# Optimization experiments

Measured on AMD Instinct MI355X. Metric: run time of the kernel, lower is better.

## Reference

```python
import jax, jax.numpy as jnp
import numpy as np
import math

H = 16
DQ = 64
NEG = -1000000000.0


def setup_inputs() -> dict:
    key = jax.random.key(0)
    ks = jax.random.split(key, 8)
    B, S, D = 2, 2048, 1024
    scale = 1.0 / math.sqrt(D)
    return {
        "embedding": jax.random.normal(ks[0], (B, S, D), dtype=jnp.float32),
        "mask": jax.random.randint(ks[1], (B, 1, S), 0, 2, dtype=jnp.int32),
        "Wq": jax.random.normal(ks[2], (D, D), dtype=jnp.float32) * scale,
        "bq": jnp.zeros((D,), dtype=jnp.float32),
        "Wk": jax.random.normal(ks[3], (D, D), dtype=jnp.float32) * scale,
        "bk": jnp.zeros((D,), dtype=jnp.float32),
        "Wv": jax.random.normal(ks[4], (D, D), dtype=jnp.float32) * scale,
        "bv": jnp.zeros((D,), dtype=jnp.float32),
        "Wo": jax.random.normal(ks[5], (D, D), dtype=jnp.float32) * scale,
        "bo": jnp.zeros((D,), dtype=jnp.float32),
    }


def reference(embedding, mask, Wq, bq, Wk, bk, Wv, bv, Wo, bo):
    B, S, D = embedding.shape
    # projections -> [B, H, S, DQ]
    def proj(W, b):
        return (embedding @ W + b).reshape(B, S, H, DQ).transpose(0, 2, 1, 3)
    q, k, v = proj(Wq, bq), proj(Wk, bk), proj(Wv, bv)
    scores = jnp.einsum("bhqd,bhkd->bhqk", q, k) / math.sqrt(DQ)
    m = mask[:, None]  # [B,1,1,S] broadcasts over heads and query positions
    scores = jnp.where(m == 0, NEG, scores)
    attn = jax.nn.softmax(scores, axis=-1)
    x = jnp.einsum("bhqk,bhkd->bhqd", attn, v)
    x = x.transpose(0, 2, 1, 3).reshape(B, S, H * DQ)
    return x @ Wo + bo
```

## Files before the change

### kernel.cpp

```cpp
#include <hip/hip_runtime.h>
#include <stdint.h>

#define B_ 2
#define S_ 2048
#define D_ 1024
#define H_ 16
#define DQ_ 64
#define M_ 4096

typedef unsigned short ushort_t;
typedef __attribute__((ext_vector_type(8))) short short8;
typedef __attribute__((ext_vector_type(4))) float floatx4;
typedef __attribute__((ext_vector_type(16))) float floatx16;

#if __has_builtin(__builtin_amdgcn_exp2f)
#define EXP2(x) __builtin_amdgcn_exp2f(x)
#else
#define EXP2(x) exp2f(x)
#endif

__device__ __forceinline__ ushort_t f2bf(float f) {
  union { float f; uint32_t u; } v; v.f = f;
  uint32_t r = v.u + 0x7FFFu + ((v.u >> 16) & 1u);
  return (ushort_t)(r >> 16);
}

__device__ __forceinline__ uint32_t pk2_trunc(float a, float b) {
  union { float f; uint32_t u; } va, vb; va.f = a; vb.f = b;
  return (va.u >> 16) | (vb.u & 0xFFFF0000u);
}
__device__ __forceinline__ uint32_t pk2_rne(float a, float b) {
  return (uint32_t)f2bf(a) | ((uint32_t)f2bf(b) << 16);
}

__device__ __forceinline__ void async16(const ushort_t* g, ushort_t* l) {
  __builtin_amdgcn_global_load_lds(
      (const __attribute__((address_space(1))) uint32_t*)g,
      (__attribute__((address_space(3))) uint32_t*)l, 16, 0, 0);
}

__global__ void k_prep(const float* __restrict__ emb, const float* __restrict__ Wq,
                       const float* __restrict__ Wk, const float* __restrict__ Wv,
                       const float* __restrict__ Wo, const int* __restrict__ mask,
                       ushort_t* __restrict__ embb, ushort_t* __restrict__ Wt,
                       int* __restrict__ pos, ushort_t* __restrict__ biasC,
                       int* __restrict__ cntp) {
  __shared__ float t[32][33];
  int blk = blockIdx.x, tid = threadIdx.x;
  if (blk < 4096) {
    int i = (blk * 256 + tid) * 4;
    float4 v = *(const float4*)(emb + i);
    uint64_t pk = (uint64_t)f2bf(v.x) | ((uint64_t)f2bf(v.y) << 16) |
                  ((uint64_t)f2bf(v.z) << 32) | ((uint64_t)f2bf(v.w) << 48);
    *(uint64_t*)(embb + i) = pk;
  } else if (blk < 8192) {
    int widx = blk - 4096;
    int z = widx >> 10, tt = widx & 1023;
    const float* W = (z == 0) ? Wq : (z == 1) ? Wk : (z == 2) ? Wv : Wo;
    ushort_t* out = Wt + (size_t)z * D_ * D_;
    int k0 = (tt >> 5) * 32, n0 = (tt & 31) * 32;
    int tx = tid & 31, ty = tid >> 5;
    for (int r = 0; r < 32; r += 8)
      t[ty + r][tx] = W[(size_t)(k0 + ty + r) * D_ + n0 + tx];
    __syncthreads();
    for (int r = 0; r < 32; r += 8)
      out[(size_t)(n0 + ty + r) * D_ + k0 + tx] = f2bf(t[tx][ty + r]);
  } else if (tid < 64) {
    int b = blk - 8192, lane = tid;
    int base = 0;
    for (int c = 0; c < 32; c++) {
      int s = c * 64 + lane;
      bool m = mask[b * S_ + s] != 0;
      unsigned long long bits = __ballot(m);
      int pre = base + __popcll(bits & ((1ull << lane) - 1ull));
      pos[b * S_ + s] = m ? pre : -1;
      base += __popcll(bits);
    }
    int cnt = base;
    for (int c = 0; c < 32; c++) {
      int i = c * 64 + lane;
      biasC[b * S_ + i] = (i < cnt) ? (ushort_t)0xC180 : (ushort_t)0xCE6E;
    }
    if (lane == 0) cntp[b] = (cnt + 63) & ~63;
  }
}

template <int IM>
__device__ __forceinline__ void gemm_core2(const ushort_t* __restrict__ A,
                                           const ushort_t* __restrict__ Bt,
                                           ushort_t* As, ushort_t* Bs,
                                           int m0, int n0, floatx4 (&acc)[IM][4]) {
  int t = threadIdx.x, lane = t & 63, w = t >> 6;
  int wm = (w >> 1) * (IM * 16), wn = (w & 1) * 64;
  int l15 = lane & 15, quad = lane >> 4;
  int srow8 = (lane >> 3) & 7;
  int sch = ((lane & 7) ^ srow8) * 8;
  const ushort_t* Ag = A + (size_t)(m0 + w * 8 + srow8) * D_ + sch;
  const ushort_t* Bg = Bt + (size_t)(n0 + w * 8 + srow8) * D_ + sch;
  for (int kt = 0; kt < D_; kt += 64) {
    __syncthreads();
#pragma unroll
    for (int c = 0; c < IM; c++)
      async16(Ag + kt + (size_t)c * 32 * D_, As + (c * 32 + w * 8) * 64);
#pragma unroll
    for (int c = 0; c < 4; c++)
      async16(Bg + kt + (size_t)c * 32 * D_, Bs + (c * 32 + w * 8) * 64);
    __syncthreads();
#pragma unroll
    for (int ks = 0; ks < 2; ks++) {
      int ch = ((ks * 4 + quad) ^ (l15 & 7)) * 8;
      short8 a[IM], b[4];
#pragma unroll
      for (int i = 0; i < IM; i++)
        a[i] = *(const short8*)(As + (wm + i * 16 + l15) * 64 + ch);
#pragma unroll
      for (int j = 0; j < 4; j++)
        b[j] = *(const short8*)(Bs + (wn + j * 16 + l15) * 64 + ch);
#pragma unroll
      for (int i = 0; i < IM; i++)
#pragma unroll
        for (int j = 0; j < 4; j++)
          acc[i][j] = __builtin_amdgcn_mfma_f32_16x16x32_bf16(a[i], b[j], acc[i][j], 0, 0, 0);
    }
  }
}

__global__ __launch_bounds__(256, 3) void k_proj(
    const ushort_t* __restrict__ A, const ushort_t* __restrict__ Wt,
    const float* __restrict__ bq, const float* __restrict__ bk,
    const float* __restrict__ bv, const int* __restrict__ pos,
    ushort_t* __restrict__ Q, ushort_t* __restrict__ K, ushort_t* __restrict__ V) {
  __shared__ __align__(16) ushort_t As[128 * 64];
  __shared__ __align__(16) ushort_t Bs[128 * 64];
  int z = blockIdx.z;
  const ushort_t* Bt = Wt + (size_t)z * D_ * D_;
  const float* bias = (z == 0) ? bq : (z == 1) ? bk : bv;
  int m0 = blockIdx.x * 128, n0 = blockIdx.y * 128;
  floatx4 acc[4][4] = {};
  gemm_core2<4>(A, Bt, As, Bs, m0, n0, acc);
  int lane = threadIdx.x & 63, w = threadIdx.x >> 6;
  int wm = (w >> 1) * 64, wn = (w & 1) * 64;
  int quad = lane >> 4, l15 = lane & 15;
  float scale = 0.125f * 1.44269504f;
#pragma unroll
  for (int i = 0; i < 4; i++)
#pragma unroll
    for (int j = 0; j < 4; j++) {
      int ncol = n0 + wn + j * 16 + l15;
      float bb = bias[ncol];
      int h = ncol >> 6, dq = ncol & 63;
      int m = m0 + wm + i * 16 + quad * 4;
      int b = m >> 11, s = m & (S_ - 1);
      if (z == 0) {
#pragma unroll
        for (int r = 0; r < 4; r++)
          Q[((size_t)(b * H_ + h) * S_ + (s + r)) * DQ_ + dq] =
              f2bf((acc[i][j][r] + bb) * scale);
      } else {
        int4 p4 = *(const int4*)(pos + b * S_ + s);
#pragma unroll
        for (int r = 0; r < 4; r++) {
          int ps = (&p4.x)[r];
          if (ps >= 0) {
            float v = acc[i][j][r] + bb;
            if (z == 1) K[((size_t)(b * H_ + h) * S_ + ps) * DQ_ + dq] = f2bf(v);
            else        V[((size_t)(b * H_ + h) * DQ_ + dq) * S_ + ps] = f2bf(v);
          }
        }
      }
    }
}

__global__ __launch_bounds__(256, 2) void k_attn(
    const ushort_t* __restrict__ Q, const ushort_t* __restrict__ Kc,
    const ushort_t* __restrict__ Vc, const ushort_t* __restrict__ biasC,
    const int* __restrict__ cntp, ushort_t* __restrict__ X) {
  int bh = blockIdx.y, b = bh >> 4, h = bh & 15;
  int t = threadIdx.x, lane = t & 63, w = t >> 6;
  int l31 = lane & 31, hi = lane >> 5;
  int q0 = blockIdx.x * 128 + w * 32;
  const ushort_t* Qh = Q + (size_t)bh * S_ * DQ_;
  const ushort_t* Kh = Kc + (size_t)bh * S_ * DQ_;
  const ushort_t* Vh = Vc + (size_t)bh * DQ_ * S_;
  const ushort_t* bbp = biasC + b * S_;
  int nk = cntp[b];

  __shared__ __align__(16) ushort_t Ks[64 * 64];
  __shared__ __align__(16) ushort_t Vs[64 * 64];

  short8 qf[4];
#pragma unroll
  for (int ks = 0; ks < 4; ks++)
    qf[ks] = *(const short8*)(Qh + (size_t)(q0 + l31) * DQ_ + ks * 16 + hi * 8);

  short8 qb = {};
  qb[0] = hi ? (short)0 : (short)0x3F80;

  int srow8 = (lane >> 3) & 7;
  int sch = ((lane & 7) ^ srow8) * 8;
  const ushort_t* Kg1 = Kh + (size_t)(w * 8 + srow8) * DQ_ + sch;
  const ushort_t* Vg1 = Vh + (size_t)(w * 8 + srow8) * S_ + sch;

  floatx16 o[2] = {};
  float lsum = 0.0f;

  for (int k0 = 0; k0 < nk; k0 += 64) {
    __syncthreads();
    async16(Kg1 + (size_t)k0 * DQ_, Ks + w * 512);
    async16(Kg1 + (size_t)(k0 + 32) * DQ_, Ks + w * 512 + 2048);
    async16(Vg1 + k0, Vs + w * 512);
    async16(Vg1 + (size_t)32 * S_ + k0, Vs + w * 512 + 2048);
    ushort_t bv0 = bbp[k0 + l31], bv1 = bbp[k0 + 32 + l31];
    __syncthreads();

    floatx16 s0 = {}, s1 = {};
#pragma unroll
    for (int ks = 0; ks < 4; ks++) {
      int ch = ((ks * 2 + hi) ^ (l31 & 7)) * 8;
      short8 kf0 = *(const short8*)(Ks + l31 * 64 + ch);
      short8 kf1 = *(const short8*)(Ks + (32 + l31) * 64 + ch);
      s0 = __builtin_amdgcn_mfma_f32_32x32x16_bf16(kf0, qf[ks], s0, 0, 0, 0);
      s1 = __builtin_amdgcn_mfma_f32_32x32x16_bf16(kf1, qf[ks], s1, 0, 0, 0);
    }
    short8 kb0 = {}, kb1 = {};
    kb0[0] = hi ? (short)0 : (short)bv0;
    kb1[0] = hi ? (short)0 : (short)bv1;
    s0 = __builtin_amdgcn_mfma_f32_32x32x16_bf16(kb0, qb, s0, 0, 0, 0);
    s1 = __builtin_amdgcn_mfma_f32_32x32x16_bf16(kb1, qb, s1, 0, 0, 0);

    uint32_t pk[2][4][2];
#pragma unroll
    for (int g = 0; g < 4; g++) {
      float p0[4], p1[4];
#pragma unroll
      for (int j = 0; j < 4; j++) {
        p0[j] = EXP2(s0[g * 4 + j]);
        p1[j] = EXP2(s1[g * 4 + j]);
        lsum += p0[j] + p1[j];
      }
      pk[0][g][0] = pk2_trunc(p0[0], p0[1]); pk[0][g][1] = pk2_trunc(p0[2], p0[3]);
      pk[1][g][0] = pk2_trunc(p1[0], p1[1]); pk[1][g][1] = pk2_trunc(p1[2], p1[3]);
    }

#pragma unroll
    for (int ks = 0; ks < 4; ks++) {
      int a = ks >> 1, gb = (ks & 1) * 2;
      uint32_t pass0 = hi ? pk[a][gb][0]     : pk[a][gb + 1][0];
      uint32_t pass1 = hi ? pk[a][gb][1]     : pk[a][gb + 1][1];
      uint32_t own0  = hi ? pk[a][gb + 1][0] : pk[a][gb][0];
      uint32_t own1  = hi ? pk[a][gb + 1][1] : pk[a][gb][1];
      uint32_t recv0 = __shfl_xor(pass0, 32, 64);
      uint32_t recv1 = __shfl_xor(pass1, 32, 64);
      union { uint32_t u[4]; short8 v; } pf;
      pf.u[0] = hi ? recv0 : own0;
      pf.u[1] = hi ? recv1 : own1;
      pf.u[2] = hi ? own0 : recv0;
      pf.u[3] = hi ? own1 : recv1;
      int ch = ((ks * 2 + hi) ^ (l31 & 7)) * 8;
      short8 vf0 = *(const short8*)(Vs + l31 * 64 + ch);
      short8 vf1 = *(const short8*)(Vs + (32 + l31) * 64 + ch);
      o[0] = __builtin_amdgcn_mfma_f32_32x32x16_bf16(vf0, pf.v, o[0], 0, 0, 0);
      o[1] = __builtin_amdgcn_mfma_f32_32x32x16_bf16(vf1, pf.v, o[1], 0, 0, 0);
    }
  }

  float l = lsum + __shfl_xor(lsum, 32, 64);
  float inv = 1.0f / l;
  int q = q0 + l31;
  size_t base = (size_t)(b * S_ + q) * D_ + h * DQ_;
#pragma unroll
  for (int a = 0; a < 2; a++)
#pragma unroll
    for (int g = 0; g < 4; g++) {
      uint2 st;
      st.x = pk2_rne(o[a][4 * g] * inv, o[a][4 * g + 1] * inv);
      st.y = pk2_rne(o[a][4 * g + 2] * inv, o[a][4 * g + 3] * inv);
      *(uint2*)(X + base + a * 32 + g * 8 + 4 * hi) = st;
    }
}

__global__ __launch_bounds__(256, 2) void k_oproj(
    const ushort_t* __restrict__ A, const ushort_t* __restrict__ Wt,
    const float* __restrict__ bias, float* __restrict__ C) {
  __shared__ __align__(16) ushort_t As[64 * 64];
  __shared__ __align__(16) ushort_t Bs[128 * 64];
  int m0 = blockIdx.x * 64, n0 = blockIdx.y * 128;
  floatx4 acc[2][4] = {};
  gemm_core2<2>(A, Wt, As, Bs, m0, n0, acc);
  int lane = threadIdx.x & 63, w = threadIdx.x >> 6;
  int wm = (w >> 1) * 32, wn = (w & 1) * 64;
  int quad = lane >> 4, l15 = lane & 15;
#pragma unroll
  for (int i = 0; i < 2; i++)
#pragma unroll
    for (int j = 0; j < 4; j++) {
      int ncol = n0 + wn + j * 16 + l15;
      float bb = bias[ncol];
      int mr = m0 + wm + i * 16 + quad * 4;
#pragma unroll
      for (int r = 0; r < 4; r++)
        C[(size_t)(mr + r) * D_ + ncol] = acc[i][j][r] + bb;
    }
}

extern "C" void kernel_launch(void* const* d_in, const int* in_sizes, int n_in,
                              void* d_out, int out_size, void* d_ws, size_t ws_size,
                              hipStream_t stream) {
  const float* emb  = (const float*)d_in[0];
  const int*   mask = (const int*)d_in[1];
  const float* Wq = (const float*)d_in[2];
  const float* bq = (const float*)d_in[3];
  const float* Wk = (const float*)d_in[4];
  const float* bk = (const float*)d_in[5];
  const float* Wv = (const float*)d_in[6];
  const float* bv = (const float*)d_in[7];
  const float* Wo = (const float*)d_in[8];
  const float* bo = (const float*)d_in[9];
  float* out = (float*)d_out;

  ushort_t* embb  = (ushort_t*)d_ws;
  ushort_t* Wt    = embb + (size_t)M_ * D_;
  ushort_t* Qb    = Wt + (size_t)4 * D_ * D_;
  ushort_t* Kb    = Qb + (size_t)M_ * D_;
  ushort_t* Vb    = Kb + (size_t)M_ * D_;
  ushort_t* Xb    = Vb + (size_t)M_ * D_;
  ushort_t* biasC = Xb + (size_t)M_ * D_;
  int* pos        = (int*)(biasC + (size_t)B_ * S_);
  int* cntp       = pos + B_ * S_;

  k_prep<<<dim3(8192 + B_), 256, 0, stream>>>(emb, Wq, Wk, Wv, Wo, mask,
                                              embb, Wt, pos, biasC, cntp);
  k_proj<<<dim3(32, 8, 3), 256, 0, stream>>>(embb, Wt, bq, bk, bv, pos, Qb, Kb, Vb);
  k_attn<<<dim3(16, 32), 256, 0, stream>>>(Qb, Kb, Vb, biasC, cntp, Xb);
  k_oproj<<<dim3(64, 8), 256, 0, stream>>>(Xb, Wt + (size_t)3 * D_ * D_, bo, out);
}
```

Before: 178.6 us.

## Fuse all four kernels into one persistent cooperative kernel with grid syncs

Replaces the prep, projection, attention and output-projection launches with a single cooperative persistent kernel. Phases are separated by grid.sync() and each phase loops over virtual blocks. The goal is to remove launch gaps and kernel-boundary drain between the four stages. In exchange, every phase runs with the fused kernel's register and LDS budget and occupancy, grid barriers cost time, and host queries (occupancy, device properties) are added on every launch.

After: 358.3 us. 101% more time.

```diff
diff --git a/kernel.cpp b/kernel.cpp
--- a/kernel.cpp
+++ b/kernel.cpp
@@ -1,4 +1,5 @@
 #include <hip/hip_runtime.h>
+#include <hip/hip_cooperative_groups.h>
 #include <stdint.h>
 
 #define B_ 2
@@ -37,52 +38,6 @@
   __builtin_amdgcn_global_load_lds(
       (const __attribute__((address_space(1))) uint32_t*)g,
       (__attribute__((address_space(3))) uint32_t*)l, 16, 0, 0);
-}
-
-__global__ void k_prep(const float* __restrict__ emb, const float* __restrict__ Wq,
-                       const float* __restrict__ Wk, const float* __restrict__ Wv,
-                       const float* __restrict__ Wo, const int* __restrict__ mask,
-                       ushort_t* __restrict__ embb, ushort_t* __restrict__ Wt,
-                       int* __restrict__ pos, ushort_t* __restrict__ biasC,
-                       int* __restrict__ cntp) {
-  __shared__ float t[32][33];
-  int blk = blockIdx.x, tid = threadIdx.x;
-  if (blk < 4096) {
-    int i = (blk * 256 + tid) * 4;
-    float4 v = *(const float4*)(emb + i);
-    uint64_t pk = (uint64_t)f2bf(v.x) | ((uint64_t)f2bf(v.y) << 16) |
-                  ((uint64_t)f2bf(v.z) << 32) | ((uint64_t)f2bf(v.w) << 48);
-    *(uint64_t*)(embb + i) = pk;
-  } else if (blk < 8192) {
-    int widx = blk - 4096;
-    int z = widx >> 10, tt = widx & 1023;
-    const float* W = (z == 0) ? Wq : (z == 1) ? Wk : (z == 2) ? Wv : Wo;
-    ushort_t* out = Wt + (size_t)z * D_ * D_;
-    int k0 = (tt >> 5) * 32, n0 = (tt & 31) * 32;
-    int tx = tid & 31, ty = tid >> 5;
-    for (int r = 0; r < 32; r += 8)
-      t[ty + r][tx] = W[(size_t)(k0 + ty + r) * D_ + n0 + tx];
-    __syncthreads();
-    for (int r = 0; r < 32; r += 8)
-      out[(size_t)(n0 + ty + r) * D_ + k0 + tx] = f2bf(t[tx][ty + r]);
-  } else if (tid < 64) {
-    int b = blk - 8192, lane = tid;
-    int base = 0;
-    for (int c = 0; c < 32; c++) {
-      int s = c * 64 + lane;
-      bool m = mask[b * S_ + s] != 0;
-      unsigned long long bits = __ballot(m);
-      int pre = base + __popcll(bits & ((1ull << lane) - 1ull));
-      pos[b * S_ + s] = m ? pre : -1;
-      base += __popcll(bits);
-    }
-    int cnt = base;
-    for (int c = 0; c < 32; c++) {
-      int i = c * 64 + lane;
-      biasC[b * S_ + i] = (i < cnt) ? (ushort_t)0xC180 : (ushort_t)0xCE6E;
-    }
-    if (lane == 0) cntp[b] = (cnt + 63) & ~63;
-  }
 }
 
 template <int IM>
@@ -125,182 +80,240 @@
   }
 }
 
-__global__ __launch_bounds__(256, 3) void k_proj(
-    const ushort_t* __restrict__ A, const ushort_t* __restrict__ Wt,
+__global__ __launch_bounds__(256, 2) void k_fused(
+    const float* __restrict__ emb, const float* __restrict__ Wq,
+    const float* __restrict__ Wk, const float* __restrict__ Wv,
+    const float* __restrict__ Wo, const int* __restrict__ mask,
     const float* __restrict__ bq, const float* __restrict__ bk,
-    const float* __restrict__ bv, const int* __restrict__ pos,
-    ushort_t* __restrict__ Q, ushort_t* __restrict__ K, ushort_t* __restrict__ V) {
-  __shared__ __align__(16) ushort_t As[128 * 64];
-  __shared__ __align__(16) ushort_t Bs[128 * 64];
-  int z = blockIdx.z;
-  const ushort_t* Bt = Wt + (size_t)z * D_ * D_;
-  const float* bias = (z == 0) ? bq : (z == 1) ? bk : bv;
-  int m0 = blockIdx.x * 128, n0 = blockIdx.y * 128;
-  floatx4 acc[4][4] = {};
-  gemm_core2<4>(A, Bt, As, Bs, m0, n0, acc);
-  int lane = threadIdx.x & 63, w = threadIdx.x >> 6;
-  int wm = (w >> 1) * 64, wn = (w & 1) * 64;
-  int quad = lane >> 4, l15 = lane & 15;
-  float scale = 0.125f * 1.44269504f;
-#pragma unroll
-  for (int i = 0; i < 4; i++)
-#pragma unroll
-    for (int j = 0; j < 4; j++) {
-      int ncol = n0 + wn + j * 16 + l15;
-      float bb = bias[ncol];
-      int h = ncol >> 6, dq = ncol & 63;
-      int m = m0 + wm + i * 16 + quad * 4;
-      int b = m >> 11, s = m & (S_ - 1);
-      if (z == 0) {
-#pragma unroll
-        for (int r = 0; r < 4; r++)
-          Q[((size_t)(b * H_ + h) * S_ + (s + r)) * DQ_ + dq] =
-              f2bf((acc[i][j][r] + bb) * scale);
-      } else {
-        int4 p4 = *(const int4*)(pos + b * S_ + s);
-#pragma unroll
-        for (int r = 0; r < 4; r++) {
-          int ps = (&p4.x)[r];
-          if (ps >= 0) {
-            float v = acc[i][j][r] + bb;
-            if (z == 1) K[((size_t)(b * H_ + h) * S_ + ps) * DQ_ + dq] = f2bf(v);
-            else        V[((size_t)(b * H_ + h) * DQ_ + dq) * S_ + ps] = f2bf(v);
+    const float* __restrict__ bv, const float* __restrict__ bo,
+    float* __restrict__ out,
+    ushort_t* __restrict__ embb, ushort_t* __restrict__ Wt,
+    ushort_t* __restrict__ Qb, ushort_t* __restrict__ Kb,
+    ushort_t* __restrict__ Vb, ushort_t* __restrict__ Xb,
+    ushort_t* __restrict__ biasC, int* __restrict__ pos,
+    int* __restrict__ cntp) {
+  cooperative_groups::grid_group grid = cooperative_groups::this_grid();
+  __shared__ __align__(16) char smem[32768];
+  int tid = threadIdx.x, nb = gridDim.x;
+  int lane = tid & 63, w = tid >> 6;
+
+  for (int vb = blockIdx.x; vb < 8192 + B_; vb += nb) {
+    if (vb < 4096) {
+      int i = (vb * 256 + tid) * 4;
+      float4 v = *(const float4*)(emb + i);
+      uint64_t pk = (uint64_t)f2bf(v.x) | ((uint64_t)f2bf(v.y) << 16) |
+                    ((uint64_t)f2bf(v.z) << 32) | ((uint64_t)f2bf(v.w) << 48);
+      *(uint64_t*)(embb + i) = pk;
+    } else if (vb < 8192) {
+      float (*t)[33] = (float(*)[33])smem;
+      int widx = vb - 4096;
+      int z = widx >> 10, tt = widx & 1023;
+      const float* W = (z == 0) ? Wq : (z == 1) ? Wk : (z == 2) ? Wv : Wo;
+      ushort_t* o = Wt + (size_t)z * D_ * D_;
+      int k0 = (tt >> 5) * 32, n0 = (tt & 31) * 32;
+      int tx = tid & 31, ty = tid >> 5;
+      __syncthreads();
+      for (int r = 0; r < 32; r += 8)
+        t[ty + r][tx] = W[(size_t)(k0 + ty + r) * D_ + n0 + tx];
+      __syncthreads();
+      for (int r = 0; r < 32; r += 8)
+        o[(size_t)(n0 + ty + r) * D_ + k0 + tx] = f2bf(t[tx][ty + r]);
+    } else if (tid < 64) {
+      int b = vb - 8192;
+      int base = 0;
+      for (int c = 0; c < 32; c++) {
+        int s = c * 64 + tid;
+        bool m = mask[b * S_ + s] != 0;
+        unsigned long long bits = __ballot(m);
+        int pre = base + __popcll(bits & ((1ull << tid) - 1ull));
+        pos[b * S_ + s] = m ? pre : -1;
+        base += __popcll(bits);
+      }
+      int cnt = base;
+      for (int c = 0; c < 32; c++) {
+        int i = c * 64 + tid;
+        biasC[b * S_ + i] = (i < cnt) ? (ushort_t)0xC180 : (ushort_t)0xCE6E;
+      }
+      if (tid == 0) cntp[b] = (cnt + 63) & ~63;
+    }
+  }
+  grid.sync();
+
+  {
+    ushort_t* As = (ushort_t*)smem;
+    ushort_t* Bs = As + 128 * 64;
+    for (int vb = blockIdx.x; vb < 768; vb += nb) {
+      int z = vb >> 8, rem = vb & 255;
+      int m0 = (rem & 31) * 128, n0 = (rem >> 5) * 128;
+      const ushort_t* Bt = Wt + (size_t)z * D_ * D_;
+      const float* bias = (z == 0) ? bq : (z == 1) ? bk : bv;
+      floatx4 acc[4][4] = {};
+      gemm_core2<4>(embb, Bt, As, Bs, m0, n0, acc);
+      int wm = (w >> 1) * 64, wn = (w & 1) * 64;
+      int quad = lane >> 4, l15 = lane & 15;
+      float scale = 0.125f * 1.44269504f;
+#pragma unroll
+      for (int i = 0; i < 4; i++)
+#pragma unroll
+        for (int j = 0; j < 4; j++) {
+          int ncol = n0 + wn + j * 16 + l15;
+          float bb = bias[ncol];
+          int h = ncol >> 6, dq = ncol & 63;
+          int m = m0 + wm + i * 16 + quad * 4;
+          int b = m >> 11, s = m & (S_ - 1);
+          if (z == 0) {
+#pragma unroll
+            for (int r = 0; r < 4; r++)
+              Qb[((size_t)(b * H_ + h) * S_ + (s + r)) * DQ_ + dq] =
+                  f2bf((acc[i][j][r] + bb) * scale);
+          } else {
+            int4 p4 = *(const int4*)(pos + b * S_ + s);
+#pragma unroll
+            for (int r = 0; r < 4; r++) {
+              int ps = (&p4.x)[r];
+              if (ps >= 0) {
+                float v = acc[i][j][r] + bb;
+                if (z == 1) Kb[((size_t)(b * H_ + h) * S_ + ps) * DQ_ + dq] = f2bf(v);
+                else        Vb[((size_t)(b * H_ + h) * DQ_ + dq) * S_ + ps] = f2bf(v);
+              }
+            }
           }
         }
+      __syncthreads();
+    }
+  }
+  grid.sync();
+
+  {
+    ushort_t* Ks = (ushort_t*)smem;
+    ushort_t* Vs = Ks + 64 * 64;
+    int l31 = lane & 31, hi = lane >> 5;
+    for (int vb = blockIdx.x; vb < 512; vb += nb) {
+      int bh = vb >> 4, b = bh >> 4, h = bh & 15;
+      int q0 = (vb & 15) * 128 + w * 32;
+      const ushort_t* Qh = Qb + (size_t)bh * S_ * DQ_;
+      const ushort_t* Kh = Kb + (size_t)bh * S_ * DQ_;
+      const ushort_t* Vh = Vb + (size_t)bh * DQ_ * S_;
+      const ushort_t* bbp = biasC + b * S_;
+      int nk = cntp[b];
+
+      short8 qf[4];
+#pragma unroll
+      for (int ks = 0; ks < 4; ks++)
+        qf[ks] = *(const short8*)(Qh + (size_t)(q0 + l31) * DQ_ + ks * 16 + hi * 8);
+      short8 qb_ = {};
+      qb_[0] = hi ? (short)0 : (short)0x3F80;
+
+      int srow8 = (lane >> 3) & 7;
+      int sch = ((lane & 7) ^ srow8) * 8;
+      const ushort_t* Kg1 = Kh + (size_t)(w * 8 + srow8) * DQ_ + sch;
+      const ushort_t* Vg1 = Vh + (size_t)(w * 8 + srow8) * S_ + sch;
+
+      floatx16 o[2] = {};
+      float lsum = 0.0f;
+
+      for (int k0 = 0; k0 < nk; k0 += 64) {
+        __syncthreads();
+        async16(Kg1 + (size_t)k0 * DQ_, Ks + w * 512);
+        async16(Kg1 + (size_t)(k0 + 32) * DQ_, Ks + w * 512 + 2048);
+        async16(Vg1 + k0, Vs + w * 512);
+        async16(Vg1 + (size_t)32 * S_ + k0, Vs + w * 512 + 2048);
+        ushort_t bv0 = bbp[k0 + l31], bv1 = bbp[k0 + 32 + l31];
+        __syncthreads();
+
+        floatx16 s0 = {}, s1 = {};
+#pragma unroll
+        for (int ks = 0; ks < 4; ks++) {
+          int ch = ((ks * 2 + hi) ^ (l31 & 7)) * 8;
+          short8 kf0 = *(const short8*)(Ks + l31 * 64 + ch);
+          short8 kf1 = *(const short8*)(Ks + (32 + l31) * 64 + ch);
+          s0 = __builtin_amdgcn_mfma_f32_32x32x16_bf16(kf0, qf[ks], s0, 0, 0, 0);
+          s1 = __builtin_amdgcn_mfma_f32_32x32x16_bf16(kf1, qf[ks], s1, 0, 0, 0);
+        }
+        short8 kb0 = {}, kb1 = {};
+        kb0[0] = hi ? (short)0 : (short)bv0;
+        kb1[0] = hi ? (short)0 : (short)bv1;
+        s0 = __builtin_amdgcn_mfma_f32_32x32x16_bf16(kb0, qb_, s0, 0, 0, 0);
+        s1 = __builtin_amdgcn_mfma_f32_32x32x16_bf16(kb1, qb_, s1, 0, 0, 0);
+
+        uint32_t pk[2][4][2];
+#pragma unroll
+        for (int g = 0; g < 4; g++) {
+          float p0[4], p1[4];
+#pragma unroll
+          for (int j = 0; j < 4; j++) {
+            p0[j] = EXP2(s0[g * 4 + j]);
+            p1[j] = EXP2(s1[g * 4 + j]);
+            lsum += p0[j] + p1[j];
+          }
+          pk[0][g][0] = pk2_trunc(p0[0], p0[1]); pk[0][g][1] = pk2_trunc(p0[2], p0[3]);
+          pk[1][g][0] = pk2_trunc(p1[0], p1[1]); pk[1][g][1] = pk2_trunc(p1[2], p1[3]);
+        }
+
+#pragma unroll
+        for (int ks = 0; ks < 4; ks++) {
+          int a = ks >> 1, gb = (ks & 1) * 2;
+          uint32_t pass0 = hi ? pk[a][gb][0]     : pk[a][gb + 1][0];
+          uint32_t pass1 = hi ? pk[a][gb][1]     : pk[a][gb + 1][1];
+          uint32_t own0  = hi ? pk[a][gb + 1][0] : pk[a][gb][0];
+          uint32_t own1  = hi ? pk[a][gb + 1][1] : pk[a][gb][1];
+          uint32_t recv0 = __shfl_xor(pass0, 32, 64);
+          uint32_t recv1 = __shfl_xor(pass1, 32, 64);
+          union { uint32_t u[4]; short8 v; } pf;
+          pf.u[0] = hi ? recv0 : own0;
+          pf.u[1] = hi ? recv1 : own1;
+          pf.u[2] = hi ? own0 : recv0;
+          pf.u[3] = hi ? own1 : recv1;
+          int ch = ((ks * 2 + hi) ^ (l31 & 7)) * 8;
+          short8 vf0 = *(const short8*)(Vs + l31 * 64 + ch);
+          short8 vf1 = *(const short8*)(Vs + (32 + l31) * 64 + ch);
+          o[0] = __builtin_amdgcn_mfma_f32_32x32x16_bf16(vf0, pf.v, o[0], 0, 0, 0);
+          o[1] = __builtin_amdgcn_mfma_f32_32x32x16_bf16(vf1, pf.v, o[1], 0, 0, 0);
+        }
       }
-    }
-}
-
-__global__ __launch_bounds__(256, 2) void k_attn(
-    const ushort_t* __restrict__ Q, const ushort_t* __restrict__ Kc,
-    const ushort_t* __restrict__ Vc, const ushort_t* __restrict__ biasC,
-    const int* __restrict__ cntp, ushort_t* __restrict__ X) {
-  int bh = blockIdx.y, b = bh >> 4, h = bh & 15;
-  int t = threadIdx.x, lane = t & 63, w = t >> 6;
-  int l31 = lane & 31, hi = lane >> 5;
-  int q0 = blockIdx.x * 128 + w * 32;
-  const ushort_t* Qh = Q + (size_t)bh * S_ * DQ_;
-  const ushort_t* Kh = Kc + (size_t)bh * S_ * DQ_;
-  const ushort_t* Vh = Vc + (size_t)bh * DQ_ * S_;
-  const ushort_t* bbp = biasC + b * S_;
-  int nk = cntp[b];
-
-  __shared__ __align__(16) ushort_t Ks[64 * 64];
-  __shared__ __align__(16) ushort_t Vs[64 * 64];
-
-  short8 qf[4];
-#pragma unroll
-  for (int ks = 0; ks < 4; ks++)
-    qf[ks] = *(const short8*)(Qh + (size_t)(q0 + l31) * DQ_ + ks * 16 + hi * 8);
-
-  short8 qb = {};
-  qb[0] = hi ? (short)0 : (short)0x3F80;
-
-  int srow8 = (lane >> 3) & 7;
-  int sch = ((lane & 7) ^ srow8) * 8;
-  const ushort_t* Kg1 = Kh + (size_t)(w * 8 + srow8) * DQ_ + sch;
-  const ushort_t* Vg1 = Vh + (size_t)(w * 8 + srow8) * S_ + sch;
-
-  floatx16 o[2] = {};
-  float lsum = 0.0f;
-
-  for (int k0 = 0; k0 < nk; k0 += 64) {
-    __syncthreads();
-    async16(Kg1 + (size_t)k0 * DQ_, Ks + w * 512);
-    async16(Kg1 + (size_t)(k0 + 32) * DQ_, Ks + w * 512 + 2048);
-    async16(Vg1 + k0, Vs + w * 512);
-    async16(Vg1 + (size_t)32 * S_ + k0, Vs + w * 512 + 2048);
-    ushort_t bv0 = bbp[k0 + l31], bv1 = bbp[k0 + 32 + l31];
-    __syncthreads();
-
-    floatx16 s0 = {}, s1 = {};
-#pragma unroll
-    for (int ks = 0; ks < 4; ks++) {
-      int ch = ((ks * 2 + hi) ^ (l31 & 7)) * 8;
-      short8 kf0 = *(const short8*)(Ks + l31 * 64 + ch);
-      short8 kf1 = *(const short8*)(Ks + (32 + l31) * 64 + ch);
-      s0 = __builtin_amdgcn_mfma_f32_32x32x16_bf16(kf0, qf[ks], s0, 0, 0, 0);
-      s1 = __builtin_amdgcn_mfma_f32_32x32x16_bf16(kf1, qf[ks], s1, 0, 0, 0);
-    }
-    short8 kb0 = {}, kb1 = {};
-    kb0[0] = hi ? (short)0 : (short)bv0;
-    kb1[0] = hi ? (short)0 : (short)bv1;
-    s0 = __builtin_amdgcn_mfma_f32_32x32x16_bf16(kb0, qb, s0, 0, 0, 0);
-    s1 = __builtin_amdgcn_mfma_f32_32x32x16_bf16(kb1, qb, s1, 0, 0, 0);
-
-    uint32_t pk[2][4][2];
-#pragma unroll
-    for (int g = 0; g < 4; g++) {
-      float p0[4], p1[4];
-#pragma unroll
-      for (int j = 0; j < 4; j++) {
-        p0[j] = EXP2(s0[g * 4 + j]);
-        p1[j] = EXP2(s1[g * 4 + j]);
-        lsum += p0[j] + p1[j];
-      }
-      pk[0][g][0] = pk2_trunc(p0[0], p0[1]); pk[0][g][1] = pk2_trunc(p0[2], p0[3]);
-      pk[1][g][0] = pk2_trunc(p1[0], p1[1]); pk[1][g][1] = pk2_trunc(p1[2], p1[3]);
-    }
-
-#pragma unroll
-    for (int ks = 0; ks < 4; ks++) {
-      int a = ks >> 1, gb = (ks & 1) * 2;
-      uint32_t pass0 = hi ? pk[a][gb][0]     : pk[a][gb + 1][0];
-      uint32_t pass1 = hi ? pk[a][gb][1]     : pk[a][gb + 1][1];
-      uint32_t own0  = hi ? pk[a][gb + 1][0] : pk[a][gb][0];
-      uint32_t own1  = hi ? pk[a][gb + 1][1] : pk[a][gb][1];
-      uint32_t recv0 = __shfl_xor(pass0, 32, 64);
-      uint32_t recv1 = __shfl_xor(pass1, 32, 64);
-      union { uint32_t u[4]; short8 v; } pf;
-      pf.u[0] = hi ? recv0 : own0;
-      pf.u[1] = hi ? recv1 : own1;
-      pf.u[2] = hi ? own0 : recv0;
-      pf.u[3] = hi ? own1 : recv1;
-      int ch = ((ks * 2 + hi) ^ (l31 & 7)) * 8;
-      short8 vf0 = *(const short8*)(Vs + l31 * 64 + ch);
-      short8 vf1 = *(const short8*)(Vs + (32 + l31) * 64 + ch);
-      o[0] = __builtin_amdgcn_mfma_f32_32x32x16_bf16(vf0, pf.v, o[0], 0, 0, 0);
-      o[1] = __builtin_amdgcn_mfma_f32_32x32x16_bf16(vf1, pf.v, o[1], 0, 0, 0);
-    }
-  }
-
-  float l = lsum + __shfl_xor(lsum, 32, 64);
-  float inv = 1.0f / l;
-  int q = q0 + l31;
-  size_t base = (size_t)(b * S_ + q) * D_ + h * DQ_;
-#pragma unroll
-  for (int a = 0; a < 2; a++)
-#pragma unroll
-    for (int g = 0; g < 4; g++) {
-      uint2 st;
-      st.x = pk2_rne(o[a][4 * g] * inv, o[a][4 * g + 1] * inv);
-      st.y = pk2_rne(o[a][4 * g + 2] * inv, o[a][4 * g + 3] * inv);
-      *(uint2*)(X + base + a * 32 + g * 8 + 4 * hi) = st;
-    }
-}
-
-__global__ __launch_bounds__(256, 2) void k_oproj(
-    const ushort_t* __restrict__ A, const ushort_t* __restrict__ Wt,
-    const float* __restrict__ bias, float* __restrict__ C) {
-  __shared__ __align__(16) ushort_t As[64 * 64];
-  __shared__ __align__(16) ushort_t Bs[128 * 64];
-  int m0 = blockIdx.x * 64, n0 = blockIdx.y * 128;
-  floatx4 acc[2][4] = {};
-  gemm_core2<2>(A, Wt, As, Bs, m0, n0, acc);
-  int lane = threadIdx.x & 63, w = threadIdx.x >> 6;
-  int wm = (w >> 1) * 32, wn = (w & 1) * 64;
-  int quad = lane >> 4, l15 = lane & 15;
-#pragma unroll
-  for (int i = 0; i < 2; i++)
-#pragma unroll
-    for (int j = 0; j < 4; j++) {
-      int ncol = n0 + wn + j * 16 + l15;
-      float bb = bias[ncol];
-      int mr = m0 + wm + i * 16 + quad * 4;
-#pragma unroll
-      for (int r = 0; r < 4; r++)
-        C[(size_t)(mr + r) * D_ + ncol] = acc[i][j][r] + bb;
-    }
+
+      float l = lsum + __shfl_xor(lsum, 32, 64);
+      float inv = 1.0f / l;
+      int q = q0 + l31;
+      size_t base = (size_t)(b * S_ + q) * D_ + h * DQ_;
+#pragma unroll
+      for (int a = 0; a < 2; a++)
+#pragma unroll
+        for (int g = 0; g < 4; g++) {
+          uint2 st;
+          st.x = pk2_rne(o[a][4 * g] * inv, o[a][4 * g + 1] * inv);
+          st.y = pk2_rne(o[a][4 * g + 2] * inv, o[a][4 * g + 3] * inv);
+          *(uint2*)(Xb + base + a * 32 + g * 8 + 4 * hi) = st;
+        }
+      __syncthreads();
+    }
+  }
+  grid.sync();
+
+  {
+    ushort_t* As = (ushort_t*)smem;
+    ushort_t* Bs = As + 64 * 64;
+    const ushort_t* Wot = Wt + (size_t)3 * D_ * D_;
+    for (int vb = blockIdx.x; vb < 512; vb += nb) {
+      int m0 = (vb & 63) * 64, n0 = (vb >> 6) * 128;
+      floatx4 acc[2][4] = {};
+      gemm_core2<2>(Xb, Wot, As, Bs, m0, n0, acc);
+      int wm = (w >> 1) * 32, wn = (w & 1) * 64;
+      int quad = lane >> 4, l15 = lane & 15;
+#pragma unroll
+      for (int i = 0; i < 2; i++)
+#pragma unroll
+        for (int j = 0; j < 4; j++) {
+          int ncol = n0 + wn + j * 16 + l15;
+          float bb = bo[ncol];
+          int mr = m0 + wm + i * 16 + quad * 4;
+#pragma unroll
+          for (int r = 0; r < 4; r++)
+            out[(size_t)(mr + r) * D_ + ncol] = acc[i][j][r] + bb;
+        }
+      __syncthreads();
+    }
+  }
 }
 
 extern "C" void kernel_launch(void* const* d_in, const int* in_sizes, int n_in,
@@ -328,9 +341,19 @@
   int* pos        = (int*)(biasC + (size_t)B_ * S_);
   int* cntp       = pos + B_ * S_;
 
-  k_prep<<<dim3(8192 + B_), 256, 0, stream>>>(emb, Wq, Wk, Wv, Wo, mask,
-                                              embb, Wt, pos, biasC, cntp);
-  k_proj<<<dim3(32, 8, 3), 256, 0, stream>>>(embb, Wt, bq, bk, bv, pos, Qb, Kb, Vb);
-  k_attn<<<dim3(16, 32), 256, 0, stream>>>(Qb, Kb, Vb, biasC, cntp, Xb);
-  k_oproj<<<dim3(64, 8), 256, 0, stream>>>(Xb, Wt + (size_t)3 * D_ * D_, bo, out);
-}
+  int bpc = 0;
+  hipOccupancyMaxActiveBlocksPerMultiprocessor(&bpc, (const void*)k_fused, 256, 0);
+  if (bpc < 1) bpc = 1;
+  if (bpc > 4) bpc = 4;
+  hipDeviceProp_t prop;
+  hipGetDeviceProperties(&prop, 0);
+  int grid = bpc * prop.multiProcessorCount;
+
+  void* args[] = {
+    (void*)&emb, (void*)&Wq, (void*)&Wk, (void*)&Wv, (void*)&Wo, (void*)&mask,
+    (void*)&bq, (void*)&bk, (void*)&bv, (void*)&bo, (void*)&out,
+    (void*)&embb, (void*)&Wt, (void*)&Qb, (void*)&Kb, (void*)&Vb, (void*)&Xb,
+    (void*)&biasC, (void*)&pos, (void*)&cntp };
+  hipLaunchCooperativeKernel((const void*)k_fused, dim3(grid), dim3(256),
+                             args, 0, stream);
+}
```
